# Kernel optimization log

Hardware: AMD Instinct MI355X
Metric: run time of the kernel (lower is better)

The kernel has to match this reference:

```python
import jax, jax.numpy as jnp
import numpy as np

# FIR kernel from resample_kernel=(1,3,3,1): outer product, normalized (gain=1)
_FIR_1D = np.array([1.0, 3.0, 3.0, 1.0], dtype=np.float32)
_FIR = np.outer(_FIR_1D, _FIR_1D)
_FIR = _FIR / _FIR.sum()  # 4x4


def setup_inputs() -> dict:
    key = jax.random.key(0)
    k1, k2, k3 = jax.random.split(key, 3)
    x = jax.random.normal(k1, (16, 256, 64, 64), dtype=jnp.float32)
    # fan_avg uniform init (default_init): variance = 1/fan_avg, fan_in=fan_out=256*9
    scale = float(np.sqrt(3.0 / (256 * 9)))
    w = jax.random.uniform(k2, (256, 256, 3, 3), dtype=jnp.float32, minval=-scale, maxval=scale)
    b = jax.random.normal(k3, (256,), dtype=jnp.float32) * 0.01
    return {"x": x, "w": w, "b": b}


def reference(x, w, b):
    # conv_downsample_2d: upfirdn2d(x, k, pad=(2,2)) then conv2d stride 2, then + bias
    B, C, H, W = x.shape
    # upfirdn2d with up=1, down=1 == zero-padded true convolution with k.
    # k is symmetric so flip is a no-op, but keep it for faithfulness.
    fir = jnp.asarray(_FIR[::-1, ::-1])                       # [4,4]
    fir_k = jnp.tile(fir[None, None, :, :], (C, 1, 1, 1))     # [C,1,4,4] depthwise
    x = jax.lax.conv_general_dilated(
        x, fir_k,
        window_strides=(1, 1),
        padding=((2, 2), (2, 2)),                             # (p+1)//2, p//2 with p=4
        feature_group_count=C,
        dimension_numbers=("NCHW", "OIHW", "NCHW"),
    )                                                          # [B,C,H+1,W+1]
    y = jax.lax.conv_general_dilated(
        x, w,
        window_strides=(2, 2),
        padding="VALID",
        dimension_numbers=("NCHW", "OIHW", "NCHW"),
    )                                                          # [B,outC,H//2,W//2]
    return y + b[None, :, None, None]
```

## Files before the change

kernel.cpp:

```cpp
#include <hip/hip_runtime.h>
#include <hip/hip_bf16.h>

typedef __attribute__((ext_vector_type(8))) short bf16x8;
typedef __attribute__((ext_vector_type(4))) float f32x4;
typedef __attribute__((ext_vector_type(8))) unsigned short u16x8;

#define KD 2304
#define PL 4232
#define OUT_PER_B (256 * 1024)

static __device__ __forceinline__ ushort f2bf(float f) {
  union { float f; unsigned int i; } v; v.f = f;
  unsigned int x = v.i;
  x += 0x7fffu + ((x >> 16) & 1u);
  return (ushort)(x >> 16);
}

#define GLDS16(gp, lp)                                                         \
  __builtin_amdgcn_global_load_lds(                                            \
      (const __attribute__((address_space(1))) void*)(gp),                     \
      (__attribute__((address_space(3))) void*)(lp), 16, 0, 0)

#define LDSOFF(p) ((unsigned)(size_t)(__attribute__((address_space(3))) const void*)(p))

#define DSREAD(dst, addr) \
  asm volatile("ds_read_b128 %0, %1" : "=v"(dst) : "v"(addr))

__global__ __launch_bounds__(256) void k_fir(const float* __restrict__ x,
                                             ushort* __restrict__ xfn,
                                             const float* __restrict__ w,
                                             ushort* __restrict__ wb) {
  __shared__ float sxp[64 * 76];
  __shared__ float stp[68 * 68];
  const int plane = blockIdx.x;
  const float* xp = x + (size_t)plane * 4096;
  ushort* op = xfn + (size_t)plane * PL;
  const int t = threadIdx.x;

  if (plane < 2304) {
    int iw = plane * 256 + t;
    float v = w[iw];
    int j = iw % 9;
    int t2 = iw / 9;
    int ic = t2 & 255;
    int oc = t2 >> 8;
    wb[oc * KD + j * 256 + ic] = f2bf(v);
  }

  {
    int r = t & 63, cs = t >> 6;
    int col = (cs < 2) ? (2 + cs) : (66 + cs);
    sxp[r * 76 + col] = 0.f;
  }
  for (int i = t; i < 272; i += 256) {
    int rr = i / 68, cc = i - rr * 68;
    int row = (rr < 2) ? rr : (64 + rr);
    stp[row * 68 + cc] = 0.f;
  }

  const float4* x4 = (const float4*)xp;
#pragma unroll
  for (int i = 0; i < 4; ++i) {
    int f4 = t + 256 * i;
    int r = f4 >> 4, w4 = f4 & 15;
    *(float4*)&sxp[r * 76 + 4 + w4 * 4] = x4[f4];
  }
  __syncthreads();

  for (int g = t; g < 1088; g += 256) {
    int i = g / 17, jg = g - i * 17;
    int j0 = jg << 2;
    const float* s = &sxp[i * 76 + j0];
    float4 a0 = *(const float4*)(s);
    float4 a1 = *(const float4*)(s + 4);
    float4 a2 = *(const float4*)(s + 8);
    float4 o;
    o.x = (a0.z + a1.y) + 3.f * (a0.w + a1.x);
    o.y = (a0.w + a1.z) + 3.f * (a1.x + a1.y);
    o.z = (a1.x + a1.w) + 3.f * (a1.y + a1.z);
    o.w = (a1.y + a2.x) + 3.f * (a1.z + a1.w);
    *(float4*)&stp[(i + 2) * 68 + j0] = o;
  }
  __syncthreads();

  for (int g = t; g < 1105; g += 256) {
    int i = g / 17, jg = g - i * 17;
    int j0 = jg << 2;
    const float* s = &stp[i * 68 + j0];
    float4 r0 = *(const float4*)(s);
    float4 r1 = *(const float4*)(s + 68);
    float4 r2 = *(const float4*)(s + 136);
    float4 r3 = *(const float4*)(s + 204);
    float4 o;
    o.x = (r0.x + r3.x) + 3.f * (r1.x + r2.x);
    o.y = (r0.y + r3.y) + 3.f * (r1.y + r2.y);
    o.z = (r0.z + r3.z) + 3.f * (r1.z + r2.z);
    o.w = (r0.w + r3.w) + 3.f * (r1.w + r2.w);
    ushort* q = op + i * 65 + j0;
    q[0] = f2bf(o.x * 0.015625f);
    if (j0 + 1 < 65) q[1] = f2bf(o.y * 0.015625f);
    if (j0 + 2 < 65) q[2] = f2bf(o.z * 0.015625f);
    if (j0 + 3 < 65) q[3] = f2bf(o.w * 0.015625f);
  }
}

__global__ __launch_bounds__(256) void k_tr(const ushort* __restrict__ xfn,
                                            ushort* __restrict__ xft) {
  __shared__ ushort ld[128 * 66];
  const int hw0 = blockIdx.x * 128;
  const int c0 = blockIdx.y * 64;
  const int b = blockIdx.z;
  const int t = threadIdx.x;

#pragma unroll
  for (int it = 0; it < 4; ++it) {
    int idx = it * 256 + t;
    int c = idx >> 4, q = idx & 15;
    u16x8 v = {};
    if (hw0 + q * 8 < 4225)
      v = *(const u16x8*)(xfn + (size_t)(b * 256 + c0 + c) * PL + hw0 + q * 8);
#pragma unroll
    for (int k = 0; k < 8; ++k)
      ld[(q * 8 + k) * 66 + (c ^ (k << 3))] = v[k];
  }
  __syncthreads();
#pragma unroll
  for (int it = 0; it < 4; ++it) {
    int idx = it * 256 + t;
    int hwl = idx >> 3, a = idx & 7;
    int k7 = hwl & 7;
    int hw = hw0 + hwl;
    if (hw < 4225) {
      u16x8 v = *(const u16x8*)&ld[hwl * 66 + ((a ^ k7) << 3)];
      *(u16x8*)&xft[((size_t)(b * 4225 + hw) << 8) + c0 + (a << 3)] = v;
    }
  }
}

__global__ __launch_bounds__(256) void k_gemm3(const ushort* __restrict__ Wb,
                                               const ushort* __restrict__ Xt,
                                               const float* __restrict__ bias,
                                               float* __restrict__ out) {
  __shared__ ushort lA[2][128 * 64];
  __shared__ ushort lB[2][128 * 64];
  const int bid = blockIdx.x;
  const int work = (bid & 7) * 32 + (bid >> 3);
  const int ntile = work >> 1;
  const int mtile = work & 1;
  const int m0 = mtile * 128;
  const int n0 = ntile * 128;
  const int t = threadIdx.x;
  const int wid = t >> 6, lane = t & 63;
  const int wm = wid >> 1, wn = wid & 1;
  const int lrow = lane & 15, kgrp = lane >> 4;

  const ushort* aB[4];
#pragma unroll
  for (int i = 0; i < 4; ++i) {
    int idx = i * 256 + t;
    int row = idx >> 3;
    aB[i] = Wb + (size_t)(m0 + row) * KD + (((idx & 7) ^ (row & 7)) << 3);
  }
  const ushort* bB[4];
#pragma unroll
  for (int i = 0; i < 4; ++i) {
    int idx = i * 256 + t;
    int row = idx >> 3;
    int n = n0 + row;
    int b = n >> 10, oh = (n >> 5) & 31, ow = n & 31;
    bB[i] = Xt + ((size_t)((b * 65 + 2 * oh) * 65 + 2 * ow) << 8) +
            (((idx & 7) ^ (row & 7)) << 3);
  }

#define STAGE(buf, kt)                                                         \
  {                                                                            \
    const int j_ = (kt) >> 2;                                                  \
    const int dh_ = j_ / 3, dw_ = j_ - 3 * dh_;                                \
    const int boff_ = (dh_ * 65 + dw_) * 256 + (((kt) & 3) << 6);              \
    const int k0_ = (kt) << 6;                                                 \
    _Pragma("unroll") for (int i_ = 0; i_ < 4; ++i_)                           \
        GLDS16(aB[i_] + k0_, &lA[buf][(i_ * 256 + t) * 8]);                    \
    _Pragma("unroll") for (int i_ = 0; i_ < 4; ++i_)                           \
        GLDS16(bB[i_] + boff_, &lB[buf][(i_ * 256 + t) * 8]);                  \
  }

  unsigned aAddr[2][4], bAddr[2][4];
#pragma unroll
  for (int f = 0; f < 4; ++f) {
    int arow = wm * 64 + f * 16 + lrow;
    int brow = wn * 64 + f * 16 + lrow;
#pragma unroll
    for (int s = 0; s < 2; ++s) {
      aAddr[s][f] = LDSOFF(&lA[0][arow * 64 + (((s * 4 + kgrp) ^ arow) & 7) * 8]);
      bAddr[s][f] = LDSOFF(&lB[0][brow * 64 + (((s * 4 + kgrp) ^ brow) & 7) * 8]);
    }
  }

  f32x4 acc[4][4];
#pragma unroll
  for (int i = 0; i < 4; ++i)
#pragma unroll
    for (int j = 0; j < 4; ++j) acc[i][j] = (f32x4){0.f, 0.f, 0.f, 0.f};

  STAGE(0, 0);

  for (int kt = 0; kt < 36; ++kt) {
    const int cur = kt & 1;
    if (kt < 35) STAGE(cur ^ 1, kt + 1);

    if (kt < 35)
      asm volatile("s_waitcnt vmcnt(8)" ::: "memory");
    else
      asm volatile("s_waitcnt vmcnt(0)" ::: "memory");
    __builtin_amdgcn_s_barrier();
    __builtin_amdgcn_sched_barrier(0);

    const unsigned off = cur ? (unsigned)(128 * 64 * 2) : 0u;
#pragma unroll
    for (int s = 0; s < 2; ++s) {
      bf16x8 Af0, Af1, Af2, Af3, Bf0, Bf1, Bf2, Bf3;
      DSREAD(Af0, aAddr[s][0] + off);
      DSREAD(Af1, aAddr[s][1] + off);
      DSREAD(Af2, aAddr[s][2] + off);
      DSREAD(Af3, aAddr[s][3] + off);
      DSREAD(Bf0, bAddr[s][0] + off);
      DSREAD(Bf1, bAddr[s][1] + off);
      DSREAD(Bf2, bAddr[s][2] + off);
      DSREAD(Bf3, bAddr[s][3] + off);
      asm volatile("s_waitcnt lgkmcnt(0)" ::: "memory");
      __builtin_amdgcn_sched_barrier(0);
      acc[0][0] = __builtin_amdgcn_mfma_f32_16x16x32_bf16(Af0, Bf0, acc[0][0], 0, 0, 0);
      acc[0][1] = __builtin_amdgcn_mfma_f32_16x16x32_bf16(Af0, Bf1, acc[0][1], 0, 0, 0);
      acc[0][2] = __builtin_amdgcn_mfma_f32_16x16x32_bf16(Af0, Bf2, acc[0][2], 0, 0, 0);
      acc[0][3] = __builtin_amdgcn_mfma_f32_16x16x32_bf16(Af0, Bf3, acc[0][3], 0, 0, 0);
      acc[1][0] = __builtin_amdgcn_mfma_f32_16x16x32_bf16(Af1, Bf0, acc[1][0], 0, 0, 0);
      acc[1][1] = __builtin_amdgcn_mfma_f32_16x16x32_bf16(Af1, Bf1, acc[1][1], 0, 0, 0);
      acc[1][2] = __builtin_amdgcn_mfma_f32_16x16x32_bf16(Af1, Bf2, acc[1][2], 0, 0, 0);
      acc[1][3] = __builtin_amdgcn_mfma_f32_16x16x32_bf16(Af1, Bf3, acc[1][3], 0, 0, 0);
      acc[2][0] = __builtin_amdgcn_mfma_f32_16x16x32_bf16(Af2, Bf0, acc[2][0], 0, 0, 0);
      acc[2][1] = __builtin_amdgcn_mfma_f32_16x16x32_bf16(Af2, Bf1, acc[2][1], 0, 0, 0);
      acc[2][2] = __builtin_amdgcn_mfma_f32_16x16x32_bf16(Af2, Bf2, acc[2][2], 0, 0, 0);
      acc[2][3] = __builtin_amdgcn_mfma_f32_16x16x32_bf16(Af2, Bf3, acc[2][3], 0, 0, 0);
      acc[3][0] = __builtin_amdgcn_mfma_f32_16x16x32_bf16(Af3, Bf0, acc[3][0], 0, 0, 0);
      acc[3][1] = __builtin_amdgcn_mfma_f32_16x16x32_bf16(Af3, Bf1, acc[3][1], 0, 0, 0);
      acc[3][2] = __builtin_amdgcn_mfma_f32_16x16x32_bf16(Af3, Bf2, acc[3][2], 0, 0, 0);
      acc[3][3] = __builtin_amdgcn_mfma_f32_16x16x32_bf16(Af3, Bf3, acc[3][3], 0, 0, 0);
    }
    __builtin_amdgcn_sched_barrier(0);
    __builtin_amdgcn_s_barrier();
  }

  f32x4 bv[4];
#pragma unroll
  for (int fm = 0; fm < 4; ++fm)
    bv[fm] = *(const f32x4*)(bias + m0 + wm * 64 + fm * 16 + kgrp * 4);

#pragma unroll
  for (int fm = 0; fm < 4; ++fm) {
#pragma unroll
    for (int fn = 0; fn < 4; ++fn) {
      int nn = n0 + wn * 64 + fn * 16 + lrow;
      int oc = m0 + wm * 64 + fm * 16 + kgrp * 4;
      float* op = out + (size_t)(nn >> 10) * OUT_PER_B + (nn & 1023) +
                  (size_t)oc * 1024;
      op[0]    = acc[fm][fn][0] + bv[fm][0];
      op[1024] = acc[fm][fn][1] + bv[fm][1];
      op[2048] = acc[fm][fn][2] + bv[fm][2];
      op[3072] = acc[fm][fn][3] + bv[fm][3];
    }
  }
}

extern "C" void kernel_launch(void* const* d_in, const int* in_sizes, int n_in,
                              void* d_out, int out_size, void* d_ws, size_t ws_size,
                              hipStream_t stream) {
  const float* x    = (const float*)d_in[0];
  const float* w    = (const float*)d_in[1];
  const float* bias = (const float*)d_in[2];
  float* out = (float*)d_out;

  char* ws = (char*)d_ws;
  ushort* xfn = (ushort*)ws;
  ushort* xft = (ushort*)(ws + 34668544);
  ushort* wb  = (ushort*)(ws + 34668544 + 34611200);

  k_fir<<<4096, 256, 0, stream>>>(x, xfn, w, wb);
  k_tr<<<dim3(34, 4, 16), 256, 0, stream>>>(xfn, xft);
  k_gemm3<<<256, 256, 0, stream>>>(wb, xft, bias, out);
}
```

Before: 69.36 us.

## Load weight fragments directly from global into registers, bypassing LDS

```diff
diff --git a/kernel.cpp b/kernel.cpp
--- a/kernel.cpp
+++ b/kernel.cpp
@@ -141,7 +141,6 @@
                                                const ushort* __restrict__ Xt,
                                                const float* __restrict__ bias,
                                                float* __restrict__ out) {
-  __shared__ ushort lA[2][128 * 64];
   __shared__ ushort lB[2][128 * 64];
   const int bid = blockIdx.x;
   const int work = (bid & 7) * 32 + (bid >> 3);
@@ -154,13 +153,6 @@
   const int wm = wid >> 1, wn = wid & 1;
   const int lrow = lane & 15, kgrp = lane >> 4;
 
-  const ushort* aB[4];
-#pragma unroll
-  for (int i = 0; i < 4; ++i) {
-    int idx = i * 256 + t;
-    int row = idx >> 3;
-    aB[i] = Wb + (size_t)(m0 + row) * KD + (((idx & 7) ^ (row & 7)) << 3);
-  }
   const ushort* bB[4];
 #pragma unroll
   for (int i = 0; i < 4; ++i) {
@@ -172,28 +164,32 @@
             (((idx & 7) ^ (row & 7)) << 3);
   }
 
+  const ushort* aP[4];
+#pragma unroll
+  for (int f = 0; f < 4; ++f)
+    aP[f] = Wb + (size_t)(m0 + wm * 64 + f * 16 + lrow) * KD + kgrp * 8;
+
 #define STAGE(buf, kt)                                                         \
   {                                                                            \
     const int j_ = (kt) >> 2;                                                  \
     const int dh_ = j_ / 3, dw_ = j_ - 3 * dh_;                                \
     const int boff_ = (dh_ * 65 + dw_) * 256 + (((kt) & 3) << 6);              \
-    const int k0_ = (kt) << 6;                                                 \
-    _Pragma("unroll") for (int i_ = 0; i_ < 4; ++i_)                           \
-        GLDS16(aB[i_] + k0_, &lA[buf][(i_ * 256 + t) * 8]);                    \
     _Pragma("unroll") for (int i_ = 0; i_ < 4; ++i_)                           \
         GLDS16(bB[i_] + boff_, &lB[buf][(i_ * 256 + t) * 8]);                  \
   }
 
-  unsigned aAddr[2][4], bAddr[2][4];
+#define ALOAD(dst, kt)                                                         \
+  _Pragma("unroll") for (int s_ = 0; s_ < 2; ++s_)                             \
+  _Pragma("unroll") for (int f_ = 0; f_ < 4; ++f_)                             \
+      dst[s_][f_] = *(const bf16x8*)(aP[f_] + (kt) * 64 + s_ * 32);
+
+  unsigned bAddr[2][4];
 #pragma unroll
   for (int f = 0; f < 4; ++f) {
-    int arow = wm * 64 + f * 16 + lrow;
     int brow = wn * 64 + f * 16 + lrow;
 #pragma unroll
-    for (int s = 0; s < 2; ++s) {
-      aAddr[s][f] = LDSOFF(&lA[0][arow * 64 + (((s * 4 + kgrp) ^ arow) & 7) * 8]);
+    for (int s = 0; s < 2; ++s)
       bAddr[s][f] = LDSOFF(&lB[0][brow * 64 + (((s * 4 + kgrp) ^ brow) & 7) * 8]);
-    }
   }
 
   f32x4 acc[4][4];
@@ -202,52 +198,58 @@
 #pragma unroll
     for (int j = 0; j < 4; ++j) acc[i][j] = (f32x4){0.f, 0.f, 0.f, 0.f};
 
+  bf16x8 Aa[2][4], Ab[2][4];
+
+#define KSTEP(kt, CUR, NXT)                                                    \
+  {                                                                            \
+    const int cur_ = (kt) & 1;                                                 \
+    if ((kt) < 35) {                                                           \
+      STAGE(cur_ ^ 1, (kt) + 1);                                               \
+      ALOAD(NXT, (kt) + 1);                                                    \
+    }                                                                          \
+    __builtin_amdgcn_sched_barrier(0);                                         \
+    if ((kt) < 35)                                                             \
+      asm volatile("s_waitcnt vmcnt(12)" ::: "memory");                        \
+    else                                                                       \
+      asm volatile("s_waitcnt vmcnt(0)" ::: "memory");                         \
+    __builtin_amdgcn_s_barrier();                                              \
+    __builtin_amdgcn_sched_barrier(0);                                         \
+    const unsigned off_ = cur_ ? (unsigned)(128 * 64 * 2) : 0u;                \
+    _Pragma("unroll") for (int s = 0; s < 2; ++s) {                            \
+      bf16x8 Bf0, Bf1, Bf2, Bf3;                                               \
+      DSREAD(Bf0, bAddr[s][0] + off_);                                         \
+      DSREAD(Bf1, bAddr[s][1] + off_);                                         \
+      DSREAD(Bf2, bAddr[s][2] + off_);                                         \
+      DSREAD(Bf3, bAddr[s][3] + off_);                                         \
+      asm volatile("s_waitcnt lgkmcnt(0)" ::: "memory");                       \
+      __builtin_amdgcn_sched_barrier(0);                                       \
+      acc[0][0] = __builtin_amdgcn_mfma_f32_16x16x32_bf16(CUR[s][0], Bf0, acc[0][0], 0, 0, 0); \
+      acc[0][1] = __builtin_amdgcn_mfma_f32_16x16x32_bf16(CUR[s][0], Bf1, acc[0][1], 0, 0, 0); \
+      acc[0][2] = __builtin_amdgcn_mfma_f32_16x16x32_bf16(CUR[s][0], Bf2, acc[0][2], 0, 0, 0); \
+      acc[0][3] = __builtin_amdgcn_mfma_f32_16x16x32_bf16(CUR[s][0], Bf3, acc[0][3], 0, 0, 0); \
+      acc[1][0] = __builtin_amdgcn_mfma_f32_16x16x32_bf16(CUR[s][1], Bf0, acc[1][0], 0, 0, 0); \
+      acc[1][1] = __builtin_amdgcn_mfma_f32_16x16x32_bf16(CUR[s][1], Bf1, acc[1][1], 0, 0, 0); \
+      acc[1][2] = __builtin_amdgcn_mfma_f32_16x16x32_bf16(CUR[s][1], Bf2, acc[1][2], 0, 0, 0); \
+      acc[1][3] = __builtin_amdgcn_mfma_f32_16x16x32_bf16(CUR[s][1], Bf3, acc[1][3], 0, 0, 0); \
+      acc[2][0] = __builtin_amdgcn_mfma_f32_16x16x32_bf16(CUR[s][2], Bf0, acc[2][0], 0, 0, 0); \
+      acc[2][1] = __builtin_amdgcn_mfma_f32_16x16x32_bf16(CUR[s][2], Bf1, acc[2][1], 0, 0, 0); \
+      acc[2][2] = __builtin_amdgcn_mfma_f32_16x16x32_bf16(CUR[s][2], Bf2, acc[2][2], 0, 0, 0); \
+      acc[2][3] = __builtin_amdgcn_mfma_f32_16x16x32_bf16(CUR[s][2], Bf3, acc[2][3], 0, 0, 0); \
+      acc[3][0] = __builtin_amdgcn_mfma_f32_16x16x32_bf16(CUR[s][3], Bf0, acc[3][0], 0, 0, 0); \
+      acc[3][1] = __builtin_amdgcn_mfma_f32_16x16x32_bf16(CUR[s][3], Bf1, acc[3][1], 0, 0, 0); \
+      acc[3][2] = __builtin_amdgcn_mfma_f32_16x16x32_bf16(CUR[s][3], Bf2, acc[3][2], 0, 0, 0); \
+      acc[3][3] = __builtin_amdgcn_mfma_f32_16x16x32_bf16(CUR[s][3], Bf3, acc[3][3], 0, 0, 0); \
+    }                                                                          \
+    __builtin_amdgcn_sched_barrier(0);                                         \
+    __builtin_amdgcn_s_barrier();                                              \
+  }
+
   STAGE(0, 0);
-
-  for (int kt = 0; kt < 36; ++kt) {
-    const int cur = kt & 1;
-    if (kt < 35) STAGE(cur ^ 1, kt + 1);
-
-    if (kt < 35)
-      asm volatile("s_waitcnt vmcnt(8)" ::: "memory");
-    else
-      asm volatile("s_waitcnt vmcnt(0)" ::: "memory");
-    __builtin_amdgcn_s_barrier();
-    __builtin_amdgcn_sched_barrier(0);
-
-    const unsigned off = cur ? (unsigned)(128 * 64 * 2) : 0u;
-#pragma unroll
-    for (int s = 0; s < 2; ++s) {
-      bf16x8 Af0, Af1, Af2, Af3, Bf0, Bf1, Bf2, Bf3;
-      DSREAD(Af0, aAddr[s][0] + off);
-      DSREAD(Af1, aAddr[s][1] + off);
-      DSREAD(Af2, aAddr[s][2] + off);
-      DSREAD(Af3, aAddr[s][3] + off);
-      DSREAD(Bf0, bAddr[s][0] + off);
-      DSREAD(Bf1, bAddr[s][1] + off);
-      DSREAD(Bf2, bAddr[s][2] + off);
-      DSREAD(Bf3, bAddr[s][3] + off);
-      asm volatile("s_waitcnt lgkmcnt(0)" ::: "memory");
-      __builtin_amdgcn_sched_barrier(0);
-      acc[0][0] = __builtin_amdgcn_mfma_f32_16x16x32_bf16(Af0, Bf0, acc[0][0], 0, 0, 0);
-      acc[0][1] = __builtin_amdgcn_mfma_f32_16x16x32_bf16(Af0, Bf1, acc[0][1], 0, 0, 0);
-      acc[0][2] = __builtin_amdgcn_mfma_f32_16x16x32_bf16(Af0, Bf2, acc[0][2], 0, 0, 0);
-      acc[0][3] = __builtin_amdgcn_mfma_f32_16x16x32_bf16(Af0, Bf3, acc[0][3], 0, 0, 0);
-      acc[1][0] = __builtin_amdgcn_mfma_f32_16x16x32_bf16(Af1, Bf0, acc[1][0], 0, 0, 0);
-      acc[1][1] = __builtin_amdgcn_mfma_f32_16x16x32_bf16(Af1, Bf1, acc[1][1], 0, 0, 0);
-      acc[1][2] = __builtin_amdgcn_mfma_f32_16x16x32_bf16(Af1, Bf2, acc[1][2], 0, 0, 0);
-      acc[1][3] = __builtin_amdgcn_mfma_f32_16x16x32_bf16(Af1, Bf3, acc[1][3], 0, 0, 0);
-      acc[2][0] = __builtin_amdgcn_mfma_f32_16x16x32_bf16(Af2, Bf0, acc[2][0], 0, 0, 0);
-      acc[2][1] = __builtin_amdgcn_mfma_f32_16x16x32_bf16(Af2, Bf1, acc[2][1], 0, 0, 0);
-      acc[2][2] = __builtin_amdgcn_mfma_f32_16x16x32_bf16(Af2, Bf2, acc[2][2], 0, 0, 0);
-      acc[2][3] = __builtin_amdgcn_mfma_f32_16x16x32_bf16(Af2, Bf3, acc[2][3], 0, 0, 0);
-      acc[3][0] = __builtin_amdgcn_mfma_f32_16x16x32_bf16(Af3, Bf0, acc[3][0], 0, 0, 0);
-      acc[3][1] = __builtin_amdgcn_mfma_f32_16x16x32_bf16(Af3, Bf1, acc[3][1], 0, 0, 0);
-      acc[3][2] = __builtin_amdgcn_mfma_f32_16x16x32_bf16(Af3, Bf2, acc[3][2], 0, 0, 0);
-      acc[3][3] = __builtin_amdgcn_mfma_f32_16x16x32_bf16(Af3, Bf3, acc[3][3], 0, 0, 0);
-    }
-    __builtin_amdgcn_sched_barrier(0);
-    __builtin_amdgcn_s_barrier();
+  ALOAD(Aa, 0);
+
+  for (int i = 0; i < 18; ++i) {
+    KSTEP(2 * i, Aa, Ab);
+    KSTEP(2 * i + 1, Ab, Aa);
   }
 
   f32x4 bv[4];
```

New measurement: 91.87 us. +32.5%, slower.
